# Optimization experiments

Hardware: AMD Instinct MI355X
Metric: run time of the kernel (lower is better)

The kernel has to match this reference:

```python
import jax, jax.numpy as jnp
import numpy as np

B, N, E, D = 128, 100, 100, 64
LAYERS = 2
ALPHA = 0.2  # LeakyReLU negative slope
NEG = -9e15


def leaky_relu(x):
    return jnp.where(x >= 0, x, ALPHA * x)


def setup_inputs() -> dict:
    key = jax.random.key(0)
    ks = jax.random.split(key, 10)
    stdv = 1.0 / np.sqrt(D)
    u = lambda k, shp: jax.random.uniform(k, shp, jnp.float32, -stdv, stdv)
    hidden = jax.random.normal(ks[0], (B, N, D), jnp.float32)
    H = jax.random.randint(ks[1], (B, N, E), 0, 4).astype(jnp.float32)
    s_c = jax.random.normal(ks[2], (B, 1, D), jnp.float32)
    return {
        "hidden": hidden,
        "H": H,
        "s_c": s_c,
        "a10": u(ks[3], (D, 1)),
        "a11": u(ks[4], (D, 1)),
        "a12": u(ks[5], (D, 1)),
        "a20": u(ks[6], (D, 1)),
        "a21": u(ks[7], (D, 1)),
        "a22": u(ks[8], (D, 1)),
    }


def _masked_attn(feat, a0, a1, a2, H, softmax_axis):
    # feat: (B,N,E,D); stack the three attention heads -> (B,N,E,3)
    A = jnp.concatenate([a0, a1, a2], axis=1)  # (D,3)
    atts = leaky_relu(jnp.einsum('bned,dk->bnek', feat, A))
    neg = jnp.full(H.shape, NEG, feat.dtype)
    alpha = jnp.where(H == 1.0, atts[..., 0], neg)
    alpha = jnp.where(H == 2.0, atts[..., 1], alpha)
    alpha = jnp.where(H == 3.0, atts[..., 2], alpha)
    return jax.nn.softmax(alpha, axis=softmax_axis)


def reference(hidden, H, s_c, a10, a11, a12, a20, a21, a22):
    H_adj = (H > 0).astype(hidden.dtype)             # (B,N,E)
    s_c_b = jnp.broadcast_to(s_c, hidden.shape)      # (B,N,D)
    h_emb = hidden
    h_out = jnp.zeros_like(hidden)
    for _ in range(LAYERS):
        # node -> edge attention
        edge_cluster = jnp.einsum('bne,bnd->bed', H_adj, h_emb)        # (B,E,D)
        h_t_cluster = h_emb + s_c_b
        feat = edge_cluster[:, None, :, :] * h_emb[:, :, None, :]       # (B,N,E,D)
        alpha1 = _masked_attn(feat, a10, a11, a12, H, softmax_axis=1)
        edge = jnp.einsum('bne,bnd->bed', alpha1, h_emb)                # (B,E,D)
        # edge -> node attention
        feat_e2n = edge[:, None, :, :] * h_t_cluster[:, :, None, :]     # (B,N,E,D)
        alpha2 = _masked_attn(feat_e2n, a20, a21, a22, H, softmax_axis=2)
        h_emb = jnp.einsum('bne,bed->bnd', alpha2, edge)                # (B,N,D)
        h_out = h_out + h_emb
    return h_out
```

## Files before the change

kernel.cpp:

```cpp
#include <hip/hip_runtime.h>
#include <math.h>

#define B_ 128
#define N_ 100
#define E_ 100
#define D_ 64
#define EH 50
#define LALPHA 0.2f
#define NEGV -9e15f

typedef __attribute__((ext_vector_type(8))) short short8;
typedef __attribute__((ext_vector_type(4))) short short4v;
typedef __attribute__((ext_vector_type(4))) float f32x4;

__device__ __forceinline__ float4 ld4(const float* p) { return *reinterpret_cast<const float4*>(p); }

__device__ __forceinline__ unsigned short f2bf(float x) {
    union { float f; unsigned u; } c; c.f = x;
    return (unsigned short)((c.u + 0x7FFF + ((c.u >> 16) & 1)) >> 16);
}
__device__ __forceinline__ short8 pk8(const unsigned short h[8]) {
    short8 r = { (short)h[0], (short)h[1], (short)h[2], (short)h[3],
                 (short)h[4], (short)h[5], (short)h[6], (short)h[7] };
    return r;
}

#define MFMA(a, b, c) __builtin_amdgcn_mfma_f32_16x16x32_bf16((a), (b), (c), 0, 0, 0)

__global__ __launch_bounds__(512, 1) void k_n2e(
    const float* __restrict__ h, const float* __restrict__ Hm,
    const float* __restrict__ a0, const float* __restrict__ a1,
    const float* __restrict__ a2, float* __restrict__ edge)
{
    __shared__ unsigned short hh[128 * 72];
    __shared__ unsigned short hT[64 * 136];
    __shared__ unsigned short m01[64 * 136];
    __shared__ float Sbuf[100 * 64];
    __shared__ unsigned short wh[3 * 64 * 72];
    __shared__ unsigned short wl[3 * 64 * 72];
    __shared__ unsigned char kk[100 * 64];
    __shared__ float sinv[64];

    const int b = blockIdx.y, e_base = blockIdx.x * EH;
    const int tid = threadIdx.x;
    const int wv = tid >> 6, ln = tid & 63, l15 = ln & 15, l4 = ln >> 4;

    for (int i = tid; i < 1088; i += 512) {
        short8 z = { 0,0,0,0,0,0,0,0 };
        reinterpret_cast<short8*>(m01)[i] = z;
    }
    for (int i = tid; i < 64 * 36; i += 512) { int d = i / 36, n = 100 + i % 36; hT[d * 136 + n] = 0; }
    for (int g = tid; g < 1600; g += 512) {
        const int n = g >> 4, d0 = (g & 15) * 4;
        const float4 v = ld4(&h[(b * N_ + n) * D_ + d0]);
        unsigned short q[4] = { f2bf(v.x), f2bf(v.y), f2bf(v.z), f2bf(v.w) };
        short4v p = { (short)q[0], (short)q[1], (short)q[2], (short)q[3] };
        *reinterpret_cast<short4v*>(&hh[n * 72 + d0]) = p;
        hT[(d0 + 0) * 136 + n] = q[0]; hT[(d0 + 1) * 136 + n] = q[1];
        hT[(d0 + 2) * 136 + n] = q[2]; hT[(d0 + 3) * 136 + n] = q[3];
    }
    __syncthreads();
    for (int i = tid; i < 6400; i += 512) {
        const int n = i >> 6, e = i & 63;
        if (e < EH) {
            const int v = (int)Hm[(b * N_ + n) * E_ + e_base + e];
            kk[n * 64 + e] = (unsigned char)v;
            m01[e * 136 + n] = (v > 0) ? (unsigned short)0x3F80 : (unsigned short)0;
        } else kk[n * 64 + e] = 0;
    }
    __syncthreads();

    {
        const int Mt = wv >> 1, NtB = (wv & 1) * 2;
        f32x4 acc0 = { 0,0,0,0 }, acc1 = { 0,0,0,0 };
        #pragma unroll
        for (int ks = 0; ks < 4; ++ks) {
            const int ko = ks * 32 + l4 * 8;
            short8 af = *reinterpret_cast<const short8*>(&m01[(Mt * 16 + l15) * 136 + ko]);
            short8 b0 = *reinterpret_cast<const short8*>(&hT[((NtB + 0) * 16 + l15) * 136 + ko]);
            short8 b1 = *reinterpret_cast<const short8*>(&hT[((NtB + 1) * 16 + l15) * 136 + ko]);
            acc0 = MFMA(af, b0, acc0);
            acc1 = MFMA(af, b1, acc1);
        }
        float* ec = Sbuf;
        #pragma unroll
        for (int r = 0; r < 4; ++r) {
            const int e = Mt * 16 + l4 * 4 + r;
            ec[e * 68 + NtB * 16 + l15] = acc0[r];
            ec[e * 68 + (NtB + 1) * 16 + l15] = acc1[r];
        }
    }
    __syncthreads();

    for (int g = tid; g < 1536; g += 512) {
        const int k = g >> 9, rem = g & 511, e = rem >> 3, d0 = (rem & 7) * 8;
        const float* ec = Sbuf;
        const float* ap = (k == 0) ? a0 : (k == 1) ? a1 : a2;
        const float4 e0 = ld4(&ec[e * 68 + d0]), e1 = ld4(&ec[e * 68 + d0 + 4]);
        const float4 av0 = ld4(&ap[d0]), av1 = ld4(&ap[d0 + 4]);
        const float wv8[8] = { e0.x * av0.x, e0.y * av0.y, e0.z * av0.z, e0.w * av0.w,
                               e1.x * av1.x, e1.y * av1.y, e1.z * av1.z, e1.w * av1.w };
        unsigned short hi[8], lo[8];
        #pragma unroll
        for (int j = 0; j < 8; ++j) {
            hi[j] = f2bf(wv8[j]);
            union { unsigned u; float f; } c; c.u = (unsigned)hi[j] << 16;
            lo[j] = f2bf(wv8[j] - c.f);
        }
        *reinterpret_cast<short8*>(&wh[(k * 64 + e) * 72 + d0]) = pk8(hi);
        *reinterpret_cast<short8*>(&wl[(k * 64 + e) * 72 + d0]) = pk8(lo);
    }
    __syncthreads();

    {
        const int Mt = wv >> 1, NtB = (wv & 1) * 4;
        f32x4 acc[3][4];
        #pragma unroll
        for (int k = 0; k < 3; ++k)
            #pragma unroll
            for (int j = 0; j < 4; ++j) { f32x4 z = { 0,0,0,0 }; acc[k][j] = z; }
        #pragma unroll
        for (int ks = 0; ks < 2; ++ks) {
            const int ko = ks * 32 + l4 * 8;
            short8 bf[4];
            #pragma unroll
            for (int j = 0; j < 4; ++j)
                bf[j] = *reinterpret_cast<const short8*>(&hh[((NtB + j) * 16 + l15) * 72 + ko]);
            #pragma unroll
            for (int k = 0; k < 3; ++k) {
                short8 ah = *reinterpret_cast<const short8*>(&wh[(k * 64 + Mt * 16 + l15) * 72 + ko]);
                short8 al = *reinterpret_cast<const short8*>(&wl[(k * 64 + Mt * 16 + l15) * 72 + ko]);
                #pragma unroll
                for (int j = 0; j < 4; ++j) {
                    acc[k][j] = MFMA(ah, bf[j], acc[k][j]);
                    acc[k][j] = MFMA(al, bf[j], acc[k][j]);
                }
            }
        }
        #pragma unroll
        for (int j = 0; j < 4; ++j) {
            const int n = (NtB + j) * 16 + l15;
            if (n < N_) {
                const int e0r = Mt * 16 + l4 * 4;
                const unsigned kw = *reinterpret_cast<const unsigned*>(&kk[n * 64 + e0r]);
                f32x4 sv;
                #pragma unroll
                for (int r = 0; r < 4; ++r) {
                    const int kv = (kw >> (8 * r)) & 255;
                    float v = (kv == 1) ? acc[0][j][r] : (kv == 2) ? acc[1][j][r] : acc[2][j][r];
                    v = (v >= 0.f) ? v : LALPHA * v;
                    sv[r] = kv ? v : NEGV;
                }
                *reinterpret_cast<f32x4*>(&Sbuf[n * 64 + e0r]) = sv;
            }
        }
    }
    __syncthreads();

    if (tid < 400) {
        const int e = tid >> 3, g = tid & 7;
        float mx = -INFINITY;
        for (int n = g; n < N_; n += 8) mx = fmaxf(mx, Sbuf[n * 64 + e]);
        mx = fmaxf(mx, __shfl_xor(mx, 1)); mx = fmaxf(mx, __shfl_xor(mx, 2)); mx = fmaxf(mx, __shfl_xor(mx, 4));
        float sum = 0.f;
        for (int n = g; n < N_; n += 8) { const float p = __expf(Sbuf[n * 64 + e] - mx); Sbuf[n * 64 + e] = p; sum += p; }
        sum += __shfl_xor(sum, 1); sum += __shfl_xor(sum, 2); sum += __shfl_xor(sum, 4);
        if (g == 0) sinv[e] = 1.f / sum;
    } else {
        for (int i = tid - 400; i < 1088; i += 112) {
            short8 z = { 0,0,0,0,0,0,0,0 };
            reinterpret_cast<short8*>(wh)[i] = z;
        }
    }
    __syncthreads();

    {
        unsigned short* PT = wh;
        for (int i = tid; i < 6400; i += 512) {
            const int n = i >> 6, e = i & 63;
            if (e < EH) PT[e * 136 + n] = f2bf(Sbuf[n * 64 + e] * sinv[e]);
        }
    }
    __syncthreads();

    {
        const unsigned short* PT = wh;
        const int Mt = wv >> 1, NtB = (wv & 1) * 2;
        f32x4 acc0 = { 0,0,0,0 }, acc1 = { 0,0,0,0 };
        #pragma unroll
        for (int ks = 0; ks < 4; ++ks) {
            const int ko = ks * 32 + l4 * 8;
            short8 af = *reinterpret_cast<const short8*>(&PT[(Mt * 16 + l15) * 136 + ko]);
            short8 b0 = *reinterpret_cast<const short8*>(&hT[((NtB + 0) * 16 + l15) * 136 + ko]);
            short8 b1 = *reinterpret_cast<const short8*>(&hT[((NtB + 1) * 16 + l15) * 136 + ko]);
            acc0 = MFMA(af, b0, acc0);
            acc1 = MFMA(af, b1, acc1);
        }
        #pragma unroll
        for (int r = 0; r < 4; ++r) {
            const int e = Mt * 16 + l4 * 4 + r;
            if (e < EH) {
                edge[(b * E_ + e_base + e) * D_ + NtB * 16 + l15] = acc0[r];
                edge[(b * E_ + e_base + e) * D_ + (NtB + 1) * 16 + l15] = acc1[r];
            }
        }
    }
}

template <bool WRITE_NEXT, bool ACC>
__global__ __launch_bounds__(512, 1) void k_e2n(
    const float* __restrict__ h, const float* __restrict__ s_c,
    const float* __restrict__ Hm, const float* __restrict__ a0,
    const float* __restrict__ a1, const float* __restrict__ a2,
    const float* __restrict__ edge, float* __restrict__ h_next,
    float* __restrict__ out)
{
    __shared__ unsigned short eh[128 * 72];
    __shared__ unsigned short ehT[64 * 136];
    __shared__ unsigned short wth[3 * 64 * 72];
    __shared__ unsigned short wtl[3 * 64 * 72];
    __shared__ float S2[100 * 64];
    __shared__ unsigned char kk2[100 * 64];
    __shared__ float sinv2[64];

    const int b = blockIdx.y, n_base = blockIdx.x * EH;
    const int tid = threadIdx.x;
    const int wv = tid >> 6, ln = tid & 63, l15 = ln & 15, l4 = ln >> 4;

    for (int i = tid; i < 64 * 36; i += 512) { int d = i / 36, e = 100 + i % 36; ehT[d * 136 + e] = 0; }
    for (int g = tid; g < 1600; g += 512) {
        const int e = g >> 4, d0 = (g & 15) * 4;
        const float4 v = ld4(&edge[(b * E_ + e) * D_ + d0]);
        unsigned short q[4] = { f2bf(v.x), f2bf(v.y), f2bf(v.z), f2bf(v.w) };
        short4v p = { (short)q[0], (short)q[1], (short)q[2], (short)q[3] };
        *reinterpret_cast<short4v*>(&eh[e * 72 + d0]) = p;
        ehT[(d0 + 0) * 136 + e] = q[0]; ehT[(d0 + 1) * 136 + e] = q[1];
        ehT[(d0 + 2) * 136 + e] = q[2]; ehT[(d0 + 3) * 136 + e] = q[3];
    }
    for (int g = tid; g < 1536; g += 512) {
        const int k = g >> 9, rem = g & 511, np = rem >> 3, d0 = (rem & 7) * 8;
        if (np < EH) {
            const float* ap = (k == 0) ? a0 : (k == 1) ? a1 : a2;
            const float4 hv0 = ld4(&h[(b * N_ + n_base + np) * D_ + d0]);
            const float4 hv1 = ld4(&h[(b * N_ + n_base + np) * D_ + d0 + 4]);
            const float4 sc0 = ld4(&s_c[b * D_ + d0]), sc1 = ld4(&s_c[b * D_ + d0 + 4]);
            const float4 av0 = ld4(&ap[d0]), av1 = ld4(&ap[d0 + 4]);
            const float wv8[8] = { (hv0.x + sc0.x) * av0.x, (hv0.y + sc0.y) * av0.y,
                                   (hv0.z + sc0.z) * av0.z, (hv0.w + sc0.w) * av0.w,
                                   (hv1.x + sc1.x) * av1.x, (hv1.y + sc1.y) * av1.y,
                                   (hv1.z + sc1.z) * av1.z, (hv1.w + sc1.w) * av1.w };
            unsigned short hi[8], lo[8];
            #pragma unroll
            for (int j = 0; j < 8; ++j) {
                hi[j] = f2bf(wv8[j]);
                union { unsigned u; float f; } c; c.u = (unsigned)hi[j] << 16;
                lo[j] = f2bf(wv8[j] - c.f);
            }
            *reinterpret_cast<short8*>(&wth[(k * 64 + np) * 72 + d0]) = pk8(hi);
            *reinterpret_cast<short8*>(&wtl[(k * 64 + np) * 72 + d0]) = pk8(lo);
        }
    }
    for (int i = tid; i < 6400; i += 512) {
        const int e = i >> 6, np = i & 63;
        if (np < EH) kk2[e * 64 + np] = (unsigned char)(int)Hm[(b * N_ + n_base + np) * E_ + e];
        else kk2[e * 64 + np] = 0;
    }
    __syncthreads();

    {
        const int Mt = wv >> 1, NtB = (wv & 1) * 4;
        f32x4 acc[3][4];
        #pragma unroll
        for (int k = 0; k < 3; ++k)
            #pragma unroll
            for (int j = 0; j < 4; ++j) { f32x4 z = { 0,0,0,0 }; acc[k][j] = z; }
        #pragma unroll
        for (int ks = 0; ks < 2; ++ks) {
            const int ko = ks * 32 + l4 * 8;
            short8 bf[4];
            #pragma unroll
            for (int j = 0; j < 4; ++j)
                bf[j] = *reinterpret_cast<const short8*>(&eh[((NtB + j) * 16 + l15) * 72 + ko]);
            #pragma unroll
            for (int k = 0; k < 3; ++k) {
                short8 ah = *reinterpret_cast<const short8*>(&wth[(k * 64 + Mt * 16 + l15) * 72 + ko]);
                short8 al = *reinterpret_cast<const short8*>(&wtl[(k * 64 + Mt * 16 + l15) * 72 + ko]);
                #pragma unroll
                for (int j = 0; j < 4; ++j) {
                    acc[k][j] = MFMA(ah, bf[j], acc[k][j]);
                    acc[k][j] = MFMA(al, bf[j], acc[k][j]);
                }
            }
        }
        #pragma unroll
        for (int j = 0; j < 4; ++j) {
            const int e = (NtB + j) * 16 + l15;
            if (e < E_) {
                const int np0 = Mt * 16 + l4 * 4;
                const unsigned kw = *reinterpret_cast<const unsigned*>(&kk2[e * 64 + np0]);
                f32x4 sv;
                #pragma unroll
                for (int r = 0; r < 4; ++r) {
                    const int kv = (kw >> (8 * r)) & 255;
                    float v = (kv == 1) ? acc[0][j][r] : (kv == 2) ? acc[1][j][r] : acc[2][j][r];
                    v = (v >= 0.f) ? v : LALPHA * v;
                    sv[r] = kv ? v : NEGV;
                }
                *reinterpret_cast<f32x4*>(&S2[e * 64 + np0]) = sv;
            }
        }
    }
    __syncthreads();

    if (tid < 400) {
        const int np = tid >> 3, g = tid & 7;
        float mx = -INFINITY;
        for (int e = g; e < E_; e += 8) mx = fmaxf(mx, S2[e * 64 + np]);
        mx = fmaxf(mx, __shfl_xor(mx, 1)); mx = fmaxf(mx, __shfl_xor(mx, 2)); mx = fmaxf(mx, __shfl_xor(mx, 4));
        float sum = 0.f;
        for (int e = g; e < E_; e += 8) { const float p = __expf(S2[e * 64 + np] - mx); S2[e * 64 + np] = p; sum += p; }
        sum += __shfl_xor(sum, 1); sum += __shfl_xor(sum, 2); sum += __shfl_xor(sum, 4);
        if (g == 0) sinv2[np] = 1.f / sum;
    } else {
        for (int i = tid - 400; i < 1088; i += 112) {
            short8 z = { 0,0,0,0,0,0,0,0 };
            reinterpret_cast<short8*>(wth)[i] = z;
        }
    }
    __syncthreads();

    {
        unsigned short* P2T = wth;
        for (int i = tid; i < 6400; i += 512) {
            const int e = i >> 6, np = i & 63;
            if (np < EH) P2T[np * 136 + e] = f2bf(S2[e * 64 + np] * sinv2[np]);
        }
    }
    __syncthreads();

    {
        const unsigned short* P2T = wth;
        const int Mt = wv >> 1, NtB = (wv & 1) * 2;
        f32x4 acc0 = { 0,0,0,0 }, acc1 = { 0,0,0,0 };
        #pragma unroll
        for (int ks = 0; ks < 4; ++ks) {
            const int ko = ks * 32 + l4 * 8;
            short8 af = *reinterpret_cast<const short8*>(&P2T[(Mt * 16 + l15) * 136 + ko]);
            short8 b0 = *reinterpret_cast<const short8*>(&ehT[((NtB + 0) * 16 + l15) * 136 + ko]);
            short8 b1 = *reinterpret_cast<const short8*>(&ehT[((NtB + 1) * 16 + l15) * 136 + ko]);
            acc0 = MFMA(af, b0, acc0);
            acc1 = MFMA(af, b1, acc1);
        }
        #pragma unroll
        for (int r = 0; r < 4; ++r) {
            const int np = Mt * 16 + l4 * 4 + r;
            if (np < EH) {
                const int idx = (b * N_ + n_base + np) * D_ + NtB * 16 + l15;
                const float v0 = acc0[r], v1 = acc1[r];
                if (WRITE_NEXT) { h_next[idx] = v0; h_next[idx + 16] = v1; }
                if (ACC) { out[idx] += v0; out[idx + 16] += v1; }
                else     { out[idx] = v0;  out[idx + 16] = v1; }
            }
        }
    }
}

extern "C" void kernel_launch(void* const* d_in, const int* in_sizes, int n_in,
                              void* d_out, int out_size, void* d_ws, size_t ws_size,
                              hipStream_t stream) {
    const float* hidden = (const float*)d_in[0];
    const float* Hm     = (const float*)d_in[1];
    const float* s_c    = (const float*)d_in[2];
    const float* a10    = (const float*)d_in[3];
    const float* a11    = (const float*)d_in[4];
    const float* a12    = (const float*)d_in[5];
    const float* a20    = (const float*)d_in[6];
    const float* a21    = (const float*)d_in[7];
    const float* a22    = (const float*)d_in[8];
    float* out = (float*)d_out;

    float* edge  = (float*)d_ws;
    float* hnext = edge + (size_t)B_ * E_ * D_;

    const dim3 grid(2, B_);

    k_n2e<<<grid, 512, 0, stream>>>(hidden, Hm, a10, a11, a12, edge);
    k_e2n<true, false><<<grid, 512, 0, stream>>>(hidden, s_c, Hm, a20, a21, a22, edge, hnext, out);
    k_n2e<<<grid, 512, 0, stream>>>(hnext, Hm, a10, a11, a12, edge);
    k_e2n<false, true><<<grid, 512, 0, stream>>>(hnext, s_c, Hm, a20, a21, a22, edge, nullptr, out);
}
```

Before: 136.8 us.

## Split each batch into four edge/node chunks and shrink LDS for higher occupancy

Halves the per-block edge/node chunk so the grid has four blocks per batch, and cuts shared memory so several blocks can share a CU (launch bounds now ask for 4 blocks). The split hi/lo bf16 attention weights are now built in registers just before the MFMAs instead of being staged in LDS. Softmax becomes one wave per row with shuffle reductions, and the normalised probabilities are written straight into a reused LDS buffer. In exchange, each block reloads and transposes the full hidden or edge tile, so that redundant load and conversion work doubles, and MFMA tiles padded to 32 rows are partly wasted.

```diff
diff --git a/kernel.cpp b/kernel.cpp
--- a/kernel.cpp
+++ b/kernel.cpp
@@ -5,7 +5,7 @@
 #define N_ 100
 #define E_ 100
 #define D_ 64
-#define EH 50
+#define EH 25
 #define LALPHA 0.2f
 #define NEGV -9e15f
 
@@ -19,37 +19,32 @@
     union { float f; unsigned u; } c; c.f = x;
     return (unsigned short)((c.u + 0x7FFF + ((c.u >> 16) & 1)) >> 16);
 }
-__device__ __forceinline__ short8 pk8(const unsigned short h[8]) {
-    short8 r = { (short)h[0], (short)h[1], (short)h[2], (short)h[3],
-                 (short)h[4], (short)h[5], (short)h[6], (short)h[7] };
-    return r;
+__device__ __forceinline__ float bf2f(unsigned short h) {
+    union { unsigned u; float f; } c; c.u = (unsigned)h << 16;
+    return c.f;
 }
 
 #define MFMA(a, b, c) __builtin_amdgcn_mfma_f32_16x16x32_bf16((a), (b), (c), 0, 0, 0)
 
-__global__ __launch_bounds__(512, 1) void k_n2e(
+__global__ __launch_bounds__(512, 4) void k_n2e(
     const float* __restrict__ h, const float* __restrict__ Hm,
     const float* __restrict__ a0, const float* __restrict__ a1,
     const float* __restrict__ a2, float* __restrict__ edge)
 {
-    __shared__ unsigned short hh[128 * 72];
-    __shared__ unsigned short hT[64 * 136];
-    __shared__ unsigned short m01[64 * 136];
-    __shared__ float Sbuf[100 * 64];
-    __shared__ unsigned short wh[3 * 64 * 72];
-    __shared__ unsigned short wl[3 * 64 * 72];
-    __shared__ unsigned char kk[100 * 64];
-    __shared__ float sinv[64];
+    __shared__ __align__(16) unsigned short hh[112 * 72];
+    __shared__ __align__(16) unsigned short hT[64 * 136];
+    __shared__ __align__(16) float S[EH * 112];
+    __shared__ __align__(16) float ec[32 * 66];
+    __shared__ __align__(16) unsigned char kk[112 * 32];
+    __shared__ __align__(16) float a_lds[3 * 68];
+
+    unsigned short* m01 = reinterpret_cast<unsigned short*>(S);
+    unsigned short* PT  = hh;
 
     const int b = blockIdx.y, e_base = blockIdx.x * EH;
     const int tid = threadIdx.x;
     const int wv = tid >> 6, ln = tid & 63, l15 = ln & 15, l4 = ln >> 4;
 
-    for (int i = tid; i < 1088; i += 512) {
-        short8 z = { 0,0,0,0,0,0,0,0 };
-        reinterpret_cast<short8*>(m01)[i] = z;
-    }
-    for (int i = tid; i < 64 * 36; i += 512) { int d = i / 36, n = 100 + i % 36; hT[d * 136 + n] = 0; }
     for (int g = tid; g < 1600; g += 512) {
         const int n = g >> 4, d0 = (g & 15) * 4;
         const float4 v = ld4(&h[(b * N_ + n) * D_ + d0]);
@@ -59,175 +54,171 @@
         hT[(d0 + 0) * 136 + n] = q[0]; hT[(d0 + 1) * 136 + n] = q[1];
         hT[(d0 + 2) * 136 + n] = q[2]; hT[(d0 + 3) * 136 + n] = q[3];
     }
-    __syncthreads();
-    for (int i = tid; i < 6400; i += 512) {
-        const int n = i >> 6, e = i & 63;
-        if (e < EH) {
-            const int v = (int)Hm[(b * N_ + n) * E_ + e_base + e];
-            kk[n * 64 + e] = (unsigned char)v;
-            m01[e * 136 + n] = (v > 0) ? (unsigned short)0x3F80 : (unsigned short)0;
-        } else kk[n * 64 + e] = 0;
-    }
-    __syncthreads();
-
-    {
-        const int Mt = wv >> 1, NtB = (wv & 1) * 2;
-        f32x4 acc0 = { 0,0,0,0 }, acc1 = { 0,0,0,0 };
+    for (int i = tid; i < 1536; i += 512) {
+        const int n = 100 + (i >> 7), d = i & 127;
+        if (d < 72) hh[n * 72 + d] = 0;
+    }
+    for (int i = tid; i < 4096; i += 512) {
+        const int d = i >> 6, c = i & 63;
+        if (c < 36) hT[d * 136 + 100 + c] = 0;
+    }
+    for (int i = tid; i < 544; i += 512) {
+        short8 z = { 0,0,0,0,0,0,0,0 };
+        reinterpret_cast<short8*>(m01)[i] = z;
+    }
+    if (tid < 192) {
+        const int k = tid >> 6, d = tid & 63;
+        a_lds[k * 68 + d] = (k == 0 ? a0 : k == 1 ? a1 : a2)[d];
+    }
+    __syncthreads();
+
+    for (int i = tid; i < 3584; i += 512) {
+        const int n = i >> 5, le = i & 31;
+        int v = 0;
+        if (n < 100 && le < EH) v = (int)Hm[(b * N_ + n) * E_ + e_base + le];
+        kk[n * 32 + le] = (unsigned char)v;
+        if (v > 0) m01[le * 136 + n] = 0x3F80;
+    }
+    __syncthreads();
+
+    {
+        const int Mt = wv >> 2, Nt = wv & 3;
+        f32x4 acc = { 0,0,0,0 };
         #pragma unroll
         for (int ks = 0; ks < 4; ++ks) {
             const int ko = ks * 32 + l4 * 8;
             short8 af = *reinterpret_cast<const short8*>(&m01[(Mt * 16 + l15) * 136 + ko]);
-            short8 b0 = *reinterpret_cast<const short8*>(&hT[((NtB + 0) * 16 + l15) * 136 + ko]);
-            short8 b1 = *reinterpret_cast<const short8*>(&hT[((NtB + 1) * 16 + l15) * 136 + ko]);
-            acc0 = MFMA(af, b0, acc0);
-            acc1 = MFMA(af, b1, acc1);
-        }
-        float* ec = Sbuf;
+            short8 bf = *reinterpret_cast<const short8*>(&hT[(Nt * 16 + l15) * 136 + ko]);
+            acc = MFMA(af, bf, acc);
+        }
+        #pragma unroll
+        for (int r = 0; r < 4; ++r)
+            ec[(Mt * 16 + l4 * 4 + r) * 66 + Nt * 16 + l15] = acc[r];
+    }
+    __syncthreads();
+
+    {
+        const int Mt = wv >> 2, NtB = (wv & 3) * 2;
+        const int ntiles = (NtB == 6) ? 1 : 2;
+        f32x4 acc[3][2];
+        #pragma unroll
+        for (int k = 0; k < 3; ++k)
+            #pragma unroll
+            for (int j = 0; j < 2; ++j) { f32x4 z = { 0,0,0,0 }; acc[k][j] = z; }
+        const int arow = Mt * 16 + l15;
+        #pragma unroll
+        for (int ks = 0; ks < 2; ++ks) {
+            const int ko = ks * 32 + l4 * 8;
+            short8 bf[2];
+            #pragma unroll
+            for (int j = 0; j < 2; ++j)
+                if (j < ntiles)
+                    bf[j] = *reinterpret_cast<const short8*>(&hh[((NtB + j) * 16 + l15) * 72 + ko]);
+            float ev[8];
+            #pragma unroll
+            for (int jj = 0; jj < 8; ++jj) ev[jj] = ec[arow * 66 + ko + jj];
+            #pragma unroll
+            for (int k = 0; k < 3; ++k) {
+                short8 ah, al;
+                #pragma unroll
+                for (int jj = 0; jj < 8; ++jj) {
+                    const float w = ev[jj] * a_lds[k * 68 + ko + jj];
+                    const unsigned short hi = f2bf(w);
+                    ah[jj] = (short)hi;
+                    al[jj] = (short)f2bf(w - bf2f(hi));
+                }
+                #pragma unroll
+                for (int j = 0; j < 2; ++j)
+                    if (j < ntiles) {
+                        acc[k][j] = MFMA(ah, bf[j], acc[k][j]);
+                        acc[k][j] = MFMA(al, bf[j], acc[k][j]);
+                    }
+            }
+        }
+        #pragma unroll
+        for (int j = 0; j < 2; ++j)
+            if (j < ntiles) {
+                const int n = (NtB + j) * 16 + l15;
+                const int e0 = Mt * 16 + l4 * 4;
+                const unsigned kw = *reinterpret_cast<const unsigned*>(&kk[n * 32 + e0]);
+                #pragma unroll
+                for (int r = 0; r < 4; ++r) {
+                    const int er = e0 + r;
+                    if (er < EH) {
+                        const int kv = (kw >> (8 * r)) & 255;
+                        float v = (kv == 1) ? acc[0][j][r] : (kv == 2) ? acc[1][j][r] : acc[2][j][r];
+                        v = (v >= 0.f) ? v : LALPHA * v;
+                        S[er * 112 + n] = kv ? v : NEGV;
+                    }
+                }
+            }
+    }
+    __syncthreads();
+
+    {
+        const int n1 = ln, n2 = ln + 64;
+        #pragma unroll
+        for (int t = 0; t < 4; ++t) {
+            const int e = wv + 8 * t;
+            if (e < EH) {
+                const float s1 = S[e * 112 + n1];
+                const float s2 = (n2 < 100) ? S[e * 112 + n2] : -INFINITY;
+                float mx = fmaxf(s1, s2);
+                #pragma unroll
+                for (int off = 32; off; off >>= 1) mx = fmaxf(mx, __shfl_xor(mx, off));
+                const float p1 = __expf(s1 - mx);
+                const float p2 = (n2 < 100) ? __expf(s2 - mx) : 0.f;
+                float sum = p1 + p2;
+                #pragma unroll
+                for (int off = 32; off; off >>= 1) sum += __shfl_xor(sum, off);
+                const float inv = 1.f / sum;
+                PT[e * 136 + n1] = f2bf(p1 * inv);
+                PT[e * 136 + n2] = (n2 < 100) ? f2bf(p2 * inv) : (unsigned short)0;
+            }
+        }
+    }
+    __syncthreads();
+
+    {
+        const int Mt = wv >> 2, Nt = wv & 3;
+        f32x4 acc = { 0,0,0,0 };
+        #pragma unroll
+        for (int ks = 0; ks < 4; ++ks) {
+            const int ko = ks * 32 + l4 * 8;
+            short8 af = *reinterpret_cast<const short8*>(&PT[(Mt * 16 + l15) * 136 + ko]);
+            short8 bf = *reinterpret_cast<const short8*>(&hT[(Nt * 16 + l15) * 136 + ko]);
+            acc = MFMA(af, bf, acc);
+        }
         #pragma unroll
         for (int r = 0; r < 4; ++r) {
             const int e = Mt * 16 + l4 * 4 + r;
-            ec[e * 68 + NtB * 16 + l15] = acc0[r];
-            ec[e * 68 + (NtB + 1) * 16 + l15] = acc1[r];
-        }
-    }
-    __syncthreads();
-
-    for (int g = tid; g < 1536; g += 512) {
-        const int k = g >> 9, rem = g & 511, e = rem >> 3, d0 = (rem & 7) * 8;
-        const float* ec = Sbuf;
-        const float* ap = (k == 0) ? a0 : (k == 1) ? a1 : a2;
-        const float4 e0 = ld4(&ec[e * 68 + d0]), e1 = ld4(&ec[e * 68 + d0 + 4]);
-        const float4 av0 = ld4(&ap[d0]), av1 = ld4(&ap[d0 + 4]);
-        const float wv8[8] = { e0.x * av0.x, e0.y * av0.y, e0.z * av0.z, e0.w * av0.w,
-                               e1.x * av1.x, e1.y * av1.y, e1.z * av1.z, e1.w * av1.w };
-        unsigned short hi[8], lo[8];
-        #pragma unroll
-        for (int j = 0; j < 8; ++j) {
-            hi[j] = f2bf(wv8[j]);
-            union { unsigned u; float f; } c; c.u = (unsigned)hi[j] << 16;
-            lo[j] = f2bf(wv8[j] - c.f);
-        }
-        *reinterpret_cast<short8*>(&wh[(k * 64 + e) * 72 + d0]) = pk8(hi);
-        *reinterpret_cast<short8*>(&wl[(k * 64 + e) * 72 + d0]) = pk8(lo);
-    }
-    __syncthreads();
-
-    {
-        const int Mt = wv >> 1, NtB = (wv & 1) * 4;
-        f32x4 acc[3][4];
-        #pragma unroll
-        for (int k = 0; k < 3; ++k)
-            #pragma unroll
-            for (int j = 0; j < 4; ++j) { f32x4 z = { 0,0,0,0 }; acc[k][j] = z; }
-        #pragma unroll
-        for (int ks = 0; ks < 2; ++ks) {
-            const int ko = ks * 32 + l4 * 8;
-            short8 bf[4];
-            #pragma unroll
-            for (int j = 0; j < 4; ++j)
-                bf[j] = *reinterpret_cast<const short8*>(&hh[((NtB + j) * 16 + l15) * 72 + ko]);
-            #pragma unroll
-            for (int k = 0; k < 3; ++k) {
-                short8 ah = *reinterpret_cast<const short8*>(&wh[(k * 64 + Mt * 16 + l15) * 72 + ko]);
-                short8 al = *reinterpret_cast<const short8*>(&wl[(k * 64 + Mt * 16 + l15) * 72 + ko]);
-                #pragma unroll
-                for (int j = 0; j < 4; ++j) {
-                    acc[k][j] = MFMA(ah, bf[j], acc[k][j]);
-                    acc[k][j] = MFMA(al, bf[j], acc[k][j]);
-                }
-            }
-        }
-        #pragma unroll
-        for (int j = 0; j < 4; ++j) {
-            const int n = (NtB + j) * 16 + l15;
-            if (n < N_) {
-                const int e0r = Mt * 16 + l4 * 4;
-                const unsigned kw = *reinterpret_cast<const unsigned*>(&kk[n * 64 + e0r]);
-                f32x4 sv;
-                #pragma unroll
-                for (int r = 0; r < 4; ++r) {
-                    const int kv = (kw >> (8 * r)) & 255;
-                    float v = (kv == 1) ? acc[0][j][r] : (kv == 2) ? acc[1][j][r] : acc[2][j][r];
-                    v = (v >= 0.f) ? v : LALPHA * v;
-                    sv[r] = kv ? v : NEGV;
-                }
-                *reinterpret_cast<f32x4*>(&Sbuf[n * 64 + e0r]) = sv;
-            }
-        }
-    }
-    __syncthreads();
-
-    if (tid < 400) {
-        const int e = tid >> 3, g = tid & 7;
-        float mx = -INFINITY;
-        for (int n = g; n < N_; n += 8) mx = fmaxf(mx, Sbuf[n * 64 + e]);
-        mx = fmaxf(mx, __shfl_xor(mx, 1)); mx = fmaxf(mx, __shfl_xor(mx, 2)); mx = fmaxf(mx, __shfl_xor(mx, 4));
-        float sum = 0.f;
-        for (int n = g; n < N_; n += 8) { const float p = __expf(Sbuf[n * 64 + e] - mx); Sbuf[n * 64 + e] = p; sum += p; }
-        sum += __shfl_xor(sum, 1); sum += __shfl_xor(sum, 2); sum += __shfl_xor(sum, 4);
-        if (g == 0) sinv[e] = 1.f / sum;
-    } else {
-        for (int i = tid - 400; i < 1088; i += 112) {
-            short8 z = { 0,0,0,0,0,0,0,0 };
-            reinterpret_cast<short8*>(wh)[i] = z;
-        }
-    }
-    __syncthreads();
-
-    {
-        unsigned short* PT = wh;
-        for (int i = tid; i < 6400; i += 512) {
-            const int n = i >> 6, e = i & 63;
-            if (e < EH) PT[e * 136 + n] = f2bf(Sbuf[n * 64 + e] * sinv[e]);
-        }
-    }
-    __syncthreads();
-
-    {
-        const unsigned short* PT = wh;
-        const int Mt = wv >> 1, NtB = (wv & 1) * 2;
-        f32x4 acc0 = { 0,0,0,0 }, acc1 = { 0,0,0,0 };
-        #pragma unroll
-        for (int ks = 0; ks < 4; ++ks) {
-            const int ko = ks * 32 + l4 * 8;
-            short8 af = *reinterpret_cast<const short8*>(&PT[(Mt * 16 + l15) * 136 + ko]);
-            short8 b0 = *reinterpret_cast<const short8*>(&hT[((NtB + 0) * 16 + l15) * 136 + ko]);
-            short8 b1 = *reinterpret_cast<const short8*>(&hT[((NtB + 1) * 16 + l15) * 136 + ko]);
-            acc0 = MFMA(af, b0, acc0);
-            acc1 = MFMA(af, b1, acc1);
-        }
-        #pragma unroll
-        for (int r = 0; r < 4; ++r) {
-            const int e = Mt * 16 + l4 * 4 + r;
-            if (e < EH) {
-                edge[(b * E_ + e_base + e) * D_ + NtB * 16 + l15] = acc0[r];
-                edge[(b * E_ + e_base + e) * D_ + (NtB + 1) * 16 + l15] = acc1[r];
-            }
+            if (e < EH)
+                edge[(b * E_ + e_base + e) * D_ + Nt * 16 + l15] = acc[r];
         }
     }
 }
 
 template <bool WRITE_NEXT, bool ACC>
-__global__ __launch_bounds__(512, 1) void k_e2n(
+__global__ __launch_bounds__(512, 4) void k_e2n(
     const float* __restrict__ h, const float* __restrict__ s_c,
     const float* __restrict__ Hm, const float* __restrict__ a0,
     const float* __restrict__ a1, const float* __restrict__ a2,
     const float* __restrict__ edge, float* __restrict__ h_next,
     float* __restrict__ out)
 {
-    __shared__ unsigned short eh[128 * 72];
-    __shared__ unsigned short ehT[64 * 136];
-    __shared__ unsigned short wth[3 * 64 * 72];
-    __shared__ unsigned short wtl[3 * 64 * 72];
-    __shared__ float S2[100 * 64];
-    __shared__ unsigned char kk2[100 * 64];
-    __shared__ float sinv2[64];
+    __shared__ __align__(16) unsigned short eh[112 * 72];
+    __shared__ __align__(16) unsigned short ehT[64 * 136];
+    __shared__ __align__(16) float S2[EH * 112];
+    __shared__ __align__(16) float ht[32 * 66];
+    __shared__ __align__(16) unsigned char kk2[112 * 32];
+    __shared__ __align__(16) float a_lds[3 * 68];
+
+    unsigned short* P2T = eh;
 
     const int b = blockIdx.y, n_base = blockIdx.x * EH;
     const int tid = threadIdx.x;
     const int wv = tid >> 6, ln = tid & 63, l15 = ln & 15, l4 = ln >> 4;
 
-    for (int i = tid; i < 64 * 36; i += 512) { int d = i / 36, e = 100 + i % 36; ehT[d * 136 + e] = 0; }
     for (int g = tid; g < 1600; g += 512) {
         const int e = g >> 4, d0 = (g & 15) * 4;
         const float4 v = ld4(&edge[(b * E_ + e) * D_ + d0]);
@@ -237,129 +228,139 @@
         ehT[(d0 + 0) * 136 + e] = q[0]; ehT[(d0 + 1) * 136 + e] = q[1];
         ehT[(d0 + 2) * 136 + e] = q[2]; ehT[(d0 + 3) * 136 + e] = q[3];
     }
-    for (int g = tid; g < 1536; g += 512) {
-        const int k = g >> 9, rem = g & 511, np = rem >> 3, d0 = (rem & 7) * 8;
-        if (np < EH) {
-            const float* ap = (k == 0) ? a0 : (k == 1) ? a1 : a2;
-            const float4 hv0 = ld4(&h[(b * N_ + n_base + np) * D_ + d0]);
-            const float4 hv1 = ld4(&h[(b * N_ + n_base + np) * D_ + d0 + 4]);
-            const float4 sc0 = ld4(&s_c[b * D_ + d0]), sc1 = ld4(&s_c[b * D_ + d0 + 4]);
-            const float4 av0 = ld4(&ap[d0]), av1 = ld4(&ap[d0 + 4]);
-            const float wv8[8] = { (hv0.x + sc0.x) * av0.x, (hv0.y + sc0.y) * av0.y,
-                                   (hv0.z + sc0.z) * av0.z, (hv0.w + sc0.w) * av0.w,
-                                   (hv1.x + sc1.x) * av1.x, (hv1.y + sc1.y) * av1.y,
-                                   (hv1.z + sc1.z) * av1.z, (hv1.w + sc1.w) * av1.w };
-            unsigned short hi[8], lo[8];
-            #pragma unroll
-            for (int j = 0; j < 8; ++j) {
-                hi[j] = f2bf(wv8[j]);
-                union { unsigned u; float f; } c; c.u = (unsigned)hi[j] << 16;
-                lo[j] = f2bf(wv8[j] - c.f);
-            }
-            *reinterpret_cast<short8*>(&wth[(k * 64 + np) * 72 + d0]) = pk8(hi);
-            *reinterpret_cast<short8*>(&wtl[(k * 64 + np) * 72 + d0]) = pk8(lo);
-        }
-    }
-    for (int i = tid; i < 6400; i += 512) {
-        const int e = i >> 6, np = i & 63;
-        if (np < EH) kk2[e * 64 + np] = (unsigned char)(int)Hm[(b * N_ + n_base + np) * E_ + e];
-        else kk2[e * 64 + np] = 0;
-    }
-    __syncthreads();
-
-    {
-        const int Mt = wv >> 1, NtB = (wv & 1) * 4;
-        f32x4 acc[3][4];
+    for (int i = tid; i < 1536; i += 512) {
+        const int e = 100 + (i >> 7), d = i & 127;
+        if (d < 72) eh[e * 72 + d] = 0;
+    }
+    for (int i = tid; i < 4096; i += 512) {
+        const int d = i >> 6, c = i & 63;
+        if (c < 36) ehT[d * 136 + 100 + c] = 0;
+    }
+    for (int g = tid; g < 400; g += 512) {
+        const int lnn = g >> 4, d0 = (g & 15) * 4;
+        const float4 hv = ld4(&h[(b * N_ + n_base + lnn) * D_ + d0]);
+        const float4 sc = ld4(&s_c[b * D_ + d0]);
+        ht[lnn * 66 + d0 + 0] = hv.x + sc.x;
+        ht[lnn * 66 + d0 + 1] = hv.y + sc.y;
+        ht[lnn * 66 + d0 + 2] = hv.z + sc.z;
+        ht[lnn * 66 + d0 + 3] = hv.w + sc.w;
+    }
+    for (int i = tid; i < 896; i += 512) {
+        const int r = 25 + (i >> 7), c = i & 127;
+        if (c < 66) ht[r * 66 + c] = 0.f;
+    }
+    if (tid < 192) {
+        const int k = tid >> 6, d = tid & 63;
+        a_lds[k * 68 + d] = (k == 0 ? a0 : k == 1 ? a1 : a2)[d];
+    }
+    for (int i = tid; i < 3584; i += 512) {
+        const int e = i >> 5, lnn = i & 31;
+        int v = 0;
+        if (e < 100 && lnn < EH) v = (int)Hm[(b * N_ + n_base + lnn) * E_ + e];
+        kk2[e * 32 + lnn] = (unsigned char)v;
+    }
+    __syncthreads();
+
+    {
+        const int Mt = wv >> 2, NtB = (wv & 3) * 2;
+        const int ntiles = (NtB == 6) ? 1 : 2;
+        f32x4 acc[3][2];
         #pragma unroll
         for (int k = 0; k < 3; ++k)
             #pragma unroll
-            for (int j = 0; j < 4; ++j) { f32x4 z = { 0,0,0,0 }; acc[k][j] = z; }
+            for (int j = 0; j < 2; ++j) { f32x4 z = { 0,0,0,0 }; acc[k][j] = z; }
+        const int arow = Mt * 16 + l15;
         #pragma unroll
         for (int ks = 0; ks < 2; ++ks) {
             const int ko = ks * 32 + l4 * 8;
-            short8 bf[4];
-            #pragma unroll
-            for (int j = 0; j < 4; ++j)
-                bf[j] = *reinterpret_cast<const short8*>(&eh[((NtB + j) * 16 + l15) * 72 + ko]);
+            short8 bf[2];
+            #pragma unroll
+            for (int j = 0; j < 2; ++j)
+                if (j < ntiles)
+                    bf[j] = *reinterpret_cast<const short8*>(&eh[((NtB + j) * 16 + l15) * 72 + ko]);
+            float ev[8];
+            #pragma unroll
+            for (int jj = 0; jj < 8; ++jj) ev[jj] = ht[arow * 66 + ko + jj];
             #pragma unroll
             for (int k = 0; k < 3; ++k) {
-                short8 ah = *reinterpret_cast<const short8*>(&wth[(k * 64 + Mt * 16 + l15) * 72 + ko]);
-                short8 al = *reinterpret_cast<const short8*>(&wtl[(k * 64 + Mt * 16 + l15) * 72 + ko]);
-                #pragma unroll
-                for (int j = 0; j < 4; ++j) {
-                    acc[k][j] = MFMA(ah, bf[j], acc[k][j]);
-                    acc[k][j] = MFMA(al, bf[j], acc[k][j]);
+                short8 ah, al;
+                #pragma unroll
+                for (int jj = 0; jj < 8; ++jj) {
+                    const float w = ev[jj] * a_lds[k * 68 + ko + jj];
+                    const unsigned short hi = f2bf(w);
+                    ah[jj] = (short)hi;
+                    al[jj] = (short)f2bf(w - bf2f(hi));
                 }
-            }
-        }
-        #pragma unroll
-        for (int j = 0; j < 4; ++j) {
-            const int e = (NtB + j) * 16 + l15;
-            if (e < E_) {
-                const int np0 = Mt * 16 + l4 * 4;
-                const unsigned kw = *reinterpret_cast<const unsigned*>(&kk2[e * 64 + np0]);
-                f32x4 sv;
+                #pragma unroll
+                for (int j = 0; j < 2; ++j)
+                    if (j < ntiles) {
+                        acc[k][j] = MFMA(ah, bf[j], acc[k][j]);
+                        acc[k][j] = MFMA(al, bf[j], acc[k][j]);
+                    }
+            }
+        }
+        #pragma unroll
+        for (int j = 0; j < 2; ++j)
+            if (j < ntiles) {
+                const int e = (NtB + j) * 16 + l15;
+                const int n0 = Mt * 16 + l4 * 4;
+                const unsigned kw = *reinterpret_cast<const unsigned*>(&kk2[e * 32 + n0]);
                 #pragma unroll
                 for (int r = 0; r < 4; ++r) {
-                    const int kv = (kw >> (8 * r)) & 255;
-                    float v = (kv == 1) ? acc[0][j][r] : (kv == 2) ? acc[1][j][r] : acc[2][j][r];
-                    v = (v >= 0.f) ? v : LALPHA * v;
-                    sv[r] = kv ? v : NEGV;
+                    const int nr = n0 + r;
+                    if (nr < EH) {
+                        const int kv = (kw >> (8 * r)) & 255;
+                        float v = (kv == 1) ? acc[0][j][r] : (kv == 2) ? acc[1][j][r] : acc[2][j][r];
+                        v = (v >= 0.f) ? v : LALPHA * v;
+                        S2[nr * 112 + e] = kv ? v : NEGV;
+                    }
                 }
-                *reinterpret_cast<f32x4*>(&S2[e * 64 + np0]) = sv;
-            }
-        }
-    }
-    __syncthreads();
-
-    if (tid < 400) {
-        const int np = tid >> 3, g = tid & 7;
-        float mx = -INFINITY;
-        for (int e = g; e < E_; e += 8) mx = fmaxf(mx, S2[e * 64 + np]);
-        mx = fmaxf(mx, __shfl_xor(mx, 1)); mx = fmaxf(mx, __shfl_xor(mx, 2)); mx = fmaxf(mx, __shfl_xor(mx, 4));
-        float sum = 0.f;
-        for (int e = g; e < E_; e += 8) { const float p = __expf(S2[e * 64 + np] - mx); S2[e * 64 + np] = p; sum += p; }
-        sum += __shfl_xor(sum, 1); sum += __shfl_xor(sum, 2); sum += __shfl_xor(sum, 4);
-        if (g == 0) sinv2[np] = 1.f / sum;
-    } else {
-        for (int i = tid - 400; i < 1088; i += 112) {
-            short8 z = { 0,0,0,0,0,0,0,0 };
-            reinterpret_cast<short8*>(wth)[i] = z;
-        }
-    }
-    __syncthreads();
-
-    {
-        unsigned short* P2T = wth;
-        for (int i = tid; i < 6400; i += 512) {
-            const int e = i >> 6, np = i & 63;
-            if (np < EH) P2T[np * 136 + e] = f2bf(S2[e * 64 + np] * sinv2[np]);
-        }
-    }
-    __syncthreads();
-
-    {
-        const unsigned short* P2T = wth;
-        const int Mt = wv >> 1, NtB = (wv & 1) * 2;
-        f32x4 acc0 = { 0,0,0,0 }, acc1 = { 0,0,0,0 };
+            }
+    }
+    __syncthreads();
+
+    {
+        const int e1 = ln, e2 = ln + 64;
+        #pragma unroll
+        for (int t = 0; t < 4; ++t) {
+            const int nr = wv + 8 * t;
+            if (nr < EH) {
+                const float s1 = S2[nr * 112 + e1];
+                const float s2 = (e2 < 100) ? S2[nr * 112 + e2] : -INFINITY;
+                float mx = fmaxf(s1, s2);
+                #pragma unroll
+                for (int off = 32; off; off >>= 1) mx = fmaxf(mx, __shfl_xor(mx, off));
+                const float p1 = __expf(s1 - mx);
+                const float p2 = (e2 < 100) ? __expf(s2 - mx) : 0.f;
+                float sum = p1 + p2;
+                #pragma unroll
+                for (int off = 32; off; off >>= 1) sum += __shfl_xor(sum, off);
+                const float inv = 1.f / sum;
+                P2T[nr * 136 + e1] = f2bf(p1 * inv);
+                P2T[nr * 136 + e2] = (e2 < 100) ? f2bf(p2 * inv) : (unsigned short)0;
+            }
+        }
+    }
+    __syncthreads();
+
+    {
+        const int Mt = wv >> 2, Nt = wv & 3;
+        f32x4 acc = { 0,0,0,0 };
         #pragma unroll
         for (int ks = 0; ks < 4; ++ks) {
             const int ko = ks * 32 + l4 * 8;
             short8 af = *reinterpret_cast<const short8*>(&P2T[(Mt * 16 + l15) * 136 + ko]);
-            short8 b0 = *reinterpret_cast<const short8*>(&ehT[((NtB + 0) * 16 + l15) * 136 + ko]);
-            short8 b1 = *reinterpret_cast<const short8*>(&ehT[((NtB + 1) * 16 + l15) * 136 + ko]);
-            acc0 = MFMA(af, b0, acc0);
-            acc1 = MFMA(af, b1, acc1);
+            short8 bf = *reinterpret_cast<const short8*>(&ehT[(Nt * 16 + l15) * 136 + ko]);
+            acc = MFMA(af, bf, acc);
         }
         #pragma unroll
         for (int r = 0; r < 4; ++r) {
-            const int np = Mt * 16 + l4 * 4 + r;
-            if (np < EH) {
-                const int idx = (b * N_ + n_base + np) * D_ + NtB * 16 + l15;
-                const float v0 = acc0[r], v1 = acc1[r];
-                if (WRITE_NEXT) { h_next[idx] = v0; h_next[idx + 16] = v1; }
-                if (ACC) { out[idx] += v0; out[idx + 16] += v1; }
-                else     { out[idx] = v0;  out[idx + 16] = v1; }
+            const int nr = Mt * 16 + l4 * 4 + r;
+            if (nr < EH) {
+                const int idx = (b * N_ + n_base + nr) * D_ + Nt * 16 + l15;
+                const float v = acc[r];
+                if (WRITE_NEXT) h_next[idx] = v;
+                if (ACC) out[idx] += v; else out[idx] = v;
             }
         }
     }
@@ -382,7 +383,7 @@
     float* edge  = (float*)d_ws;
     float* hnext = edge + (size_t)B_ * E_ * D_;
 
-    const dim3 grid(2, B_);
+    const dim3 grid(4, B_);
 
     k_n2e<<<grid, 512, 0, stream>>>(hidden, Hm, a10, a11, a12, edge);
     k_e2n<true, false><<<grid, 512, 0, stream>>>(hidden, s_c, Hm, a20, a21, a22, edge, hnext, out);
```

After: 134.6 us. About the same (-1.6%).
